# Kernel tuning notes

Hardware: AMD Instinct MI355X
Metric: run time of the kernel (lower is better)

Reference implementation:

```python
import jax, jax.numpy as jnp
import numpy as np

TEMP = 0.07  # init temperature
EPS = 1e-12  # F.normalize eps


def _per_cloud_loss(fmap, labels):
    # fmap: [C, N] per-point features; labels: [N] int
    v = fmap.T  # [N, C]
    v = v / jnp.maximum(jnp.linalg.norm(v, axis=1, keepdims=True), EPS)
    # NxN similarity, exp then divide by temp (order matches original)
    dot = jnp.exp(v @ v.T) / TEMP  # [N, N]
    dot = dot - jnp.diag(jnp.diag(dot))  # zero the diagonal
    mask = (labels[:, None] == labels[None, :]).astype(dot.dtype)  # [N, N]
    mask_not = 1.0 - mask
    pos = (mask * dot).sum(1) / mask.sum(1)  # note: denom includes self, as in original
    neg = (mask_not * dot).sum(1) / mask_not.sum(1)
    return jnp.mean(-jnp.log(pos / (pos + neg)))


def setup_inputs() -> dict:
    key = jax.random.key(0)
    k1, k2 = jax.random.split(key)
    B, C, N = 8, 128, 4096
    features = jax.random.normal(k1, (B, C, N), dtype=jnp.float32)
    labels_all = jax.random.randint(k2, (B, N), 0, 16, dtype=jnp.int64)
    return {"features": features, "labels_all": labels_all}


def reference(features, labels_all):
    losses = jax.vmap(_per_cloud_loss)(features, labels_all)  # [B]
    return jnp.mean(losses)
```

## Files before the change

### kernel.cpp

```cpp
#include <hip/hip_runtime.h>
#include <stdint.h>

#define NPTS 4096
#define NC 128
#define NB 8
#define CSPLIT 8
#define COLS_PER (NPTS / CSPLIT)
#define RPB 128

typedef __bf16 bf16x8 __attribute__((ext_vector_type(8)));
typedef float f32x4 __attribute__((ext_vector_type(4)));
typedef unsigned short u16;
typedef unsigned int u32;

__device__ inline float fast_exp2(float x) { return __builtin_amdgcn_exp2f(x); }

__device__ inline u16 f2bf(float x) {
    u32 u = __float_as_uint(x);
    u32 r = (u + 0x7fffu + ((u >> 16) & 1u)) >> 16;
    return (u16)r;
}

__global__ __launch_bounds__(256) void norm_count_kernel(const float* __restrict__ feat,
                                                         const int* __restrict__ labels,
                                                         u16* __restrict__ vbf,
                                                         int* __restrict__ counts,
                                                         u32* __restrict__ zbase) {
    int b = blockIdx.y;
    int tid = threadIdx.x;
    if (blockIdx.x == 64) {
        if (b == 0 && tid < 2) zbase[tid] = 0u;
        __shared__ int h[16];
        if (tid < 16) h[tid] = 0;
        __syncthreads();
        for (int n = tid; n < NPTS; n += 256)
            atomicAdd(&h[labels[b * NPTS + n] & 15], 1);
        __syncthreads();
        if (tid < 16) counts[b * 16 + tid] = h[tid];
        return;
    }
    int n0 = blockIdx.x * 64;
    __shared__ float tile[64][129];
    __shared__ float part[8][64];
    __shared__ float rn[64];
    const float* fb = feat + (size_t)b * NC * NPTS;
    int nslot = tid & 31;
    int ty = tid >> 5;
    float s0 = 0.f, s1 = 0.f;
#pragma unroll
    for (int i = 0; i < 16; ++i) {
        int c = i * 8 + ty;
        float2 x = *(const float2*)(fb + (size_t)c * NPTS + n0 + 2 * nslot);
        tile[2 * nslot][c] = x.x;
        tile[2 * nslot + 1][c] = x.y;
        s0 += x.x * x.x;
        s1 += x.y * x.y;
    }
    part[ty][2 * nslot] = s0;
    part[ty][2 * nslot + 1] = s1;
    __syncthreads();
    if (tid < 64) {
        float s = 0.f;
#pragma unroll
        for (int t = 0; t < 8; ++t) s += part[t][tid];
        rn[tid] = 1.f / fmaxf(sqrtf(s), 1e-12f);
    }
    __syncthreads();
    u32* out = (u32*)vbf;
    size_t obase = ((size_t)b * NPTS + n0) * (NC / 2);
#pragma unroll
    for (int i = 0; i < 16; ++i) {
        int idx = tid + i * 256;
        int p = idx >> 6, k = idx & 63;
        float r = rn[p];
        float x0 = tile[p][2 * k] * r;
        float x1 = tile[p][2 * k + 1] * r;
        out[obase + (size_t)p * 64 + k] = (u32)f2bf(x0) | ((u32)f2bf(x1) << 16);
    }
}

__global__ __launch_bounds__(256, 2) void sim_kernel(const u16* __restrict__ vbf,
                                                     const int* __restrict__ labels,
                                                     float2* __restrict__ rowacc) {
    int bid = blockIdx.x;
    int rt = bid >> 6;
    int combo = bid & 63;
    int b = combo >> 3;
    int cs = combo & 7;
    int row0 = rt * RPB;
    int c0 = cs * COLS_PER;
    int tid = threadIdx.x;
    int wave = tid >> 6, lane = tid & 63;
    int quad = lane >> 4, ln = lane & 15;

    const u16* vb = vbf + (size_t)b * NPTS * NC;
    const int* lab = labels + b * NPTS;

    int rbase[2];
    rbase[0] = row0 + wave * 32;
    rbase[1] = rbase[0] + 16;

    bf16x8 afrag[2][4];
#pragma unroll
    for (int s = 0; s < 2; ++s)
#pragma unroll
        for (int f = 0; f < 4; ++f) {
            bf16x8 v = *(const bf16x8*)(vb + (size_t)(rbase[s] + ln) * NC + f * 32 + quad * 8);
#pragma unroll
            for (int k = 0; k < 8; ++k) v[k] = (__bf16)((float)v[k] * 1.44269504f);
            afrag[s][f] = v;
        }

    int lrow[2][4];
#pragma unroll
    for (int s = 0; s < 2; ++s)
#pragma unroll
        for (int r = 0; r < 4; ++r) lrow[s][r] = lab[rbase[s] + quad * 4 + r];

    int diagct[2], diagsub[2];
#pragma unroll
    for (int s = 0; s < 2; ++s) {
        diagct[s] = rbase[s] & ~63;
        diagsub[s] = (rbase[s] >> 4) & 3;
    }

    float psame[2][4] = {{0.f}}, sall[2][4] = {{0.f}};

    __shared__ u16 cols[64 * 128];
    __shared__ int clab[64];

    const uint4* src = (const uint4*)(vb + (size_t)c0 * NC);
    u32 woff[4];
#pragma unroll
    for (int i = 0; i < 4; ++i) {
        int idx = tid + i * 256;
        int rr = idx >> 4, cc = idx & 15;
        woff[i] = rr * 128 + ((cc ^ (rr & 15)) * 8);
    }

    for (int t = 0; t < COLS_PER / 64; ++t) {
        int ct = c0 + t * 64;
        __syncthreads();
#pragma unroll
        for (int i = 0; i < 4; ++i)
            *(uint4*)(cols + woff[i]) = src[t * 1024 + tid + i * 256];
        if (tid < 64) clab[tid] = lab[ct + tid];
        __syncthreads();

#pragma unroll
        for (int sub = 0; sub < 4; ++sub) {
            const u16* rowb = cols + (sub * 16 + ln) * 128;
            bf16x8 bfrag[4];
#pragma unroll
            for (int f = 0; f < 4; ++f)
                bfrag[f] = *(const bf16x8*)(rowb + (((4 * f + quad) ^ ln) * 8));
            int lc = clab[sub * 16 + ln];
#pragma unroll
            for (int s = 0; s < 2; ++s) {
                f32x4 d = {0.f, 0.f, 0.f, 0.f};
#pragma unroll
                for (int f = 0; f < 4; ++f)
                    d = __builtin_amdgcn_mfma_f32_16x16x32_bf16(afrag[s][f], bfrag[f], d, 0, 0, 0);
                if (ct == diagct[s] && sub == diagsub[s]) {
#pragma unroll
                    for (int r = 0; r < 4; ++r) {
                        float e = fast_exp2(d[r]);
                        if (ln == quad * 4 + r) e = 0.f;
                        sall[s][r] += e;
                        psame[s][r] += (lc == lrow[s][r]) ? e : 0.f;
                    }
                } else {
#pragma unroll
                    for (int r = 0; r < 4; ++r) {
                        float e = fast_exp2(d[r]);
                        sall[s][r] += e;
                        psame[s][r] += (lc == lrow[s][r]) ? e : 0.f;
                    }
                }
            }
        }
    }

#pragma unroll
    for (int off = 1; off < 16; off <<= 1)
#pragma unroll
        for (int s = 0; s < 2; ++s)
#pragma unroll
            for (int r = 0; r < 4; ++r) {
                psame[s][r] += __shfl_xor(psame[s][r], off);
                sall[s][r] += __shfl_xor(sall[s][r], off);
            }
    if (ln == 0) {
#pragma unroll
        for (int s = 0; s < 2; ++s)
#pragma unroll
            for (int r = 0; r < 4; ++r)
                rowacc[((size_t)cs * NB + b) * NPTS + rbase[s] + quad * 4 + r] =
                    make_float2(psame[s][r], sall[s][r]);
    }
}

__global__ __launch_bounds__(256) void loss_kernel(const float2* __restrict__ rowacc,
                                                   const int* __restrict__ labels,
                                                   const int* __restrict__ counts,
                                                   float* __restrict__ acc,
                                                   u32* __restrict__ ticket,
                                                   float* __restrict__ out) {
    int idx = blockIdx.x * 256 + threadIdx.x;
    int b = idx >> 12;
    float ps = 0.f, sa = 0.f;
#pragma unroll
    for (int cs = 0; cs < CSPLIT; ++cs) {
        float2 v = rowacc[(size_t)cs * NB * NPTS + idx];
        ps += v.x;
        sa += v.y;
    }
    int lb = labels[idx] & 15;
    int cnt = counts[b * 16 + lb];
    float p = ps / (float)cnt;
    float n = (sa - ps) / (float)(NPTS - cnt);
    float loss = -__logf(p / (p + n));
#pragma unroll
    for (int off = 1; off < 64; off <<= 1) loss += __shfl_xor(loss, off);
    __shared__ float w[4];
    if ((threadIdx.x & 63) == 0) w[threadIdx.x >> 6] = loss;
    __syncthreads();
    if (threadIdx.x == 0) {
        atomicAdd(acc, w[0] + w[1] + w[2] + w[3]);
        __threadfence();
        u32 t = atomicAdd(ticket, 1u);
        if (t == gridDim.x - 1) {
            float v = atomicAdd(acc, 0.f);
            out[0] = v * (1.f / (float)(NB * NPTS));
        }
    }
}

extern "C" void kernel_launch(void* const* d_in, const int* in_sizes, int n_in,
                              void* d_out, int out_size, void* d_ws, size_t ws_size,
                              hipStream_t stream) {
    const float* feat = (const float*)d_in[0];
    const int* labels = (const int*)d_in[1];
    float* out = (float*)d_out;

    float* acc = (float*)d_ws;
    u32* ticket = (u32*)((char*)d_ws + 4);
    int* counts = (int*)((char*)d_ws + 256);
    float2* rowacc = (float2*)((char*)d_ws + 4096);
    u16* vbf = (u16*)((char*)d_ws + 4096 + (size_t)CSPLIT * NB * NPTS * 8);

    norm_count_kernel<<<dim3(65, NB), 256, 0, stream>>>(feat, labels, vbf, counts, (u32*)d_ws);
    sim_kernel<<<dim3(32 * 64), 256, 0, stream>>>(vbf, labels, rowacc);
    loss_kernel<<<dim3(NB * NPTS / 256), 256, 0, stream>>>(rowacc, labels, counts, acc, ticket, out);
}
```

Measured before the change: 131.1 us.

## Sort points by label, add uniform-tile fast path, double-buffer column loads

Adds a histogram/prefix kernel and scatters normalized features into label-sorted order, so most 16x16 tiles have uniform row and column labels. For those tiles the per-element compare and select is replaced by a single branch. Column tiles are now loaded straight into double-buffered LDS with global_load_lds, prefetching the next tile during compute, and the per-tile syncthreads drops from two to one. The kernel accumulates positive and negative sums separately instead of total minus positive, at the cost of an extra launch and a scattered write.

```diff
diff --git a/kernel.cpp b/kernel.cpp
--- a/kernel.cpp
+++ b/kernel.cpp
@@ -12,6 +12,7 @@
 typedef float f32x4 __attribute__((ext_vector_type(4)));
 typedef unsigned short u16;
 typedef unsigned int u32;
+typedef unsigned long long u64;
 
 __device__ inline float fast_exp2(float x) { return __builtin_amdgcn_exp2f(x); }
 
@@ -21,28 +22,59 @@
     return (u16)r;
 }
 
-__global__ __launch_bounds__(256) void norm_count_kernel(const float* __restrict__ feat,
-                                                         const int* __restrict__ labels,
-                                                         u16* __restrict__ vbf,
-                                                         int* __restrict__ counts,
-                                                         u32* __restrict__ zbase) {
+typedef __attribute__((address_space(1))) const void glb_void;
+typedef __attribute__((address_space(3))) void lds_void;
+__device__ inline void gload_lds16(const void* g, void* l) {
+    __builtin_amdgcn_global_load_lds((glb_void*)g, (lds_void*)l, 16, 0, 0);
+}
+
+__global__ __launch_bounds__(256) void hist_kernel(const int* __restrict__ labels,
+                                                   int* __restrict__ counts,
+                                                   int* __restrict__ baseg,
+                                                   u32* __restrict__ zb) {
+    int b = blockIdx.x, tid = threadIdx.x;
+    if (b == 0 && tid < 2) zb[tid] = 0u;
+    __shared__ int cnt[64][16];
+    __shared__ int tot[16];
+    for (int i = tid; i < 64 * 16; i += 256) ((int*)cnt)[i] = 0;
+    __syncthreads();
+    for (int n = tid; n < NPTS; n += 256)
+        atomicAdd(&cnt[n >> 6][labels[b * NPTS + n] & 15], 1);
+    __syncthreads();
+    if (tid < 16) {
+        int s = 0;
+        for (int k = 0; k < 64; ++k) s += cnt[k][tid];
+        counts[b * 16 + tid] = s;
+        tot[tid] = s;
+    }
+    __syncthreads();
+    if (tid == 0) {
+        int run = 0;
+        for (int l = 0; l < 16; ++l) { int c = tot[l]; tot[l] = run; run += c; }
+    }
+    __syncthreads();
+    if (tid < 16) {
+        int run = tot[tid];
+        for (int k = 0; k < 64; ++k) {
+            baseg[(b * 64 + k) * 16 + tid] = run;
+            run += cnt[k][tid];
+        }
+    }
+}
+
+__global__ __launch_bounds__(256) void norm_kernel(const float* __restrict__ feat,
+                                                   const int* __restrict__ labels,
+                                                   const int* __restrict__ baseg,
+                                                   u16* __restrict__ vbf,
+                                                   int* __restrict__ slab) {
     int b = blockIdx.y;
+    int blk = blockIdx.x;
     int tid = threadIdx.x;
-    if (blockIdx.x == 64) {
-        if (b == 0 && tid < 2) zbase[tid] = 0u;
-        __shared__ int h[16];
-        if (tid < 16) h[tid] = 0;
-        __syncthreads();
-        for (int n = tid; n < NPTS; n += 256)
-            atomicAdd(&h[labels[b * NPTS + n] & 15], 1);
-        __syncthreads();
-        if (tid < 16) counts[b * 16 + tid] = h[tid];
-        return;
-    }
-    int n0 = blockIdx.x * 64;
+    int n0 = blk * 64;
     __shared__ float tile[64][129];
     __shared__ float part[8][64];
     __shared__ float rn[64];
+    __shared__ int lpos[64];
     const float* fb = feat + (size_t)b * NC * NPTS;
     int nslot = tid & 31;
     int ty = tid >> 5;
@@ -64,10 +96,20 @@
 #pragma unroll
         for (int t = 0; t < 8; ++t) s += part[t][tid];
         rn[tid] = 1.f / fmaxf(sqrtf(s), 1e-12f);
+        int myl = labels[b * NPTS + n0 + tid] & 15;
+        u64 mymask = 0ull;
+#pragma unroll
+        for (int L = 0; L < 16; ++L) {
+            u64 bl = __ballot(myl == L);
+            if (myl == L) mymask = bl;
+        }
+        int rank = __popcll(mymask & ((1ull << tid) - 1ull));
+        int pos = baseg[(b * 64 + blk) * 16 + myl] + rank;
+        lpos[tid] = pos;
+        slab[b * NPTS + pos] = myl;
     }
     __syncthreads();
     u32* out = (u32*)vbf;
-    size_t obase = ((size_t)b * NPTS + n0) * (NC / 2);
 #pragma unroll
     for (int i = 0; i < 16; ++i) {
         int idx = tid + i * 256;
@@ -75,12 +117,12 @@
         float r = rn[p];
         float x0 = tile[p][2 * k] * r;
         float x1 = tile[p][2 * k + 1] * r;
-        out[obase + (size_t)p * 64 + k] = (u32)f2bf(x0) | ((u32)f2bf(x1) << 16);
+        out[((size_t)b * NPTS + lpos[p]) * 64 + k] = (u32)f2bf(x0) | ((u32)f2bf(x1) << 16);
     }
 }
 
 __global__ __launch_bounds__(256, 2) void sim_kernel(const u16* __restrict__ vbf,
-                                                     const int* __restrict__ labels,
+                                                     const int* __restrict__ slab,
                                                      float2* __restrict__ rowacc) {
     int bid = blockIdx.x;
     int rt = bid >> 6;
@@ -94,7 +136,7 @@
     int quad = lane >> 4, ln = lane & 15;
 
     const u16* vb = vbf + (size_t)b * NPTS * NC;
-    const int* lab = labels + b * NPTS;
+    const int* lab = slab + b * NPTS;
 
     int rbase[2];
     rbase[0] = row0 + wave * 32;
@@ -117,6 +159,10 @@
 #pragma unroll
         for (int r = 0; r < 4; ++r) lrow[s][r] = lab[rbase[s] + quad * 4 + r];
 
+    int row_uni[2];
+#pragma unroll
+    for (int s = 0; s < 2; ++s) row_uni[s] = (lab[rbase[s]] == lab[rbase[s] + 15]);
+
     int diagct[2], diagsub[2];
 #pragma unroll
     for (int s = 0; s < 2; ++s) {
@@ -124,37 +170,46 @@
         diagsub[s] = (rbase[s] >> 4) & 3;
     }
 
-    float psame[2][4] = {{0.f}}, sall[2][4] = {{0.f}};
-
-    __shared__ u16 cols[64 * 128];
-    __shared__ int clab[64];
+    float psame[2][4] = {{0.f}}, pneg[2][4] = {{0.f}};
+
+    __shared__ u16 cols[2][64 * 128];
+    __shared__ int clabs[512];
+    clabs[tid] = lab[c0 + tid];
+    clabs[tid + 256] = lab[c0 + 256 + tid];
 
     const uint4* src = (const uint4*)(vb + (size_t)c0 * NC);
-    u32 woff[4];
+    int g4[4];
 #pragma unroll
     for (int i = 0; i < 4; ++i) {
-        int idx = tid + i * 256;
-        int rr = idx >> 4, cc = idx & 15;
-        woff[i] = rr * 128 + ((cc ^ (rr & 15)) * 8);
-    }
+        int idx16 = (wave * 4 + i) * 64 + lane;
+        int rr = idx16 >> 4;
+        int cc = (idx16 & 15) ^ (rr & 15);
+        g4[i] = rr * 16 + cc;
+    }
+
+    int cur = 0;
+#pragma unroll
+    for (int i = 0; i < 4; ++i)
+        gload_lds16(src + g4[i], cols[0] + (wave * 4 + i) * 512);
 
     for (int t = 0; t < COLS_PER / 64; ++t) {
+        __syncthreads();
+        if (t < COLS_PER / 64 - 1) {
+#pragma unroll
+            for (int i = 0; i < 4; ++i)
+                gload_lds16(src + (t + 1) * 1024 + g4[i], cols[cur ^ 1] + (wave * 4 + i) * 512);
+        }
         int ct = c0 + t * 64;
-        __syncthreads();
-#pragma unroll
-        for (int i = 0; i < 4; ++i)
-            *(uint4*)(cols + woff[i]) = src[t * 1024 + tid + i * 256];
-        if (tid < 64) clab[tid] = lab[ct + tid];
-        __syncthreads();
 
 #pragma unroll
         for (int sub = 0; sub < 4; ++sub) {
-            const u16* rowb = cols + (sub * 16 + ln) * 128;
+            const u16* rowb = cols[cur] + (sub * 16 + ln) * 128;
             bf16x8 bfrag[4];
 #pragma unroll
             for (int f = 0; f < 4; ++f)
                 bfrag[f] = *(const bf16x8*)(rowb + (((4 * f + quad) ^ ln) * 8));
-            int lc = clab[sub * 16 + ln];
+            int lc = clabs[t * 64 + sub * 16 + ln];
+            int clo = __shfl(lc, 0), chi = __shfl(lc, 15);
 #pragma unroll
             for (int s = 0; s < 2; ++s) {
                 f32x4 d = {0.f, 0.f, 0.f, 0.f};
@@ -166,19 +221,30 @@
                     for (int r = 0; r < 4; ++r) {
                         float e = fast_exp2(d[r]);
                         if (ln == quad * 4 + r) e = 0.f;
-                        sall[s][r] += e;
-                        psame[s][r] += (lc == lrow[s][r]) ? e : 0.f;
+                        bool m = (lc == lrow[s][r]);
+                        psame[s][r] += m ? e : 0.f;
+                        pneg[s][r] += m ? 0.f : e;
+                    }
+                } else if (row_uni[s] && clo == chi) {
+                    if (clo == lrow[s][0]) {
+#pragma unroll
+                        for (int r = 0; r < 4; ++r) psame[s][r] += fast_exp2(d[r]);
+                    } else {
+#pragma unroll
+                        for (int r = 0; r < 4; ++r) pneg[s][r] += fast_exp2(d[r]);
                     }
                 } else {
 #pragma unroll
                     for (int r = 0; r < 4; ++r) {
                         float e = fast_exp2(d[r]);
-                        sall[s][r] += e;
-                        psame[s][r] += (lc == lrow[s][r]) ? e : 0.f;
+                        bool m = (lc == lrow[s][r]);
+                        psame[s][r] += m ? e : 0.f;
+                        pneg[s][r] += m ? 0.f : e;
                     }
                 }
             }
         }
+        cur ^= 1;
     }
 
 #pragma unroll
@@ -188,7 +254,7 @@
 #pragma unroll
             for (int r = 0; r < 4; ++r) {
                 psame[s][r] += __shfl_xor(psame[s][r], off);
-                sall[s][r] += __shfl_xor(sall[s][r], off);
+                pneg[s][r] += __shfl_xor(pneg[s][r], off);
             }
     if (ln == 0) {
 #pragma unroll
@@ -196,29 +262,29 @@
 #pragma unroll
             for (int r = 0; r < 4; ++r)
                 rowacc[((size_t)cs * NB + b) * NPTS + rbase[s] + quad * 4 + r] =
-                    make_float2(psame[s][r], sall[s][r]);
+                    make_float2(psame[s][r], pneg[s][r]);
     }
 }
 
 __global__ __launch_bounds__(256) void loss_kernel(const float2* __restrict__ rowacc,
-                                                   const int* __restrict__ labels,
+                                                   const int* __restrict__ slab,
                                                    const int* __restrict__ counts,
                                                    float* __restrict__ acc,
                                                    u32* __restrict__ ticket,
                                                    float* __restrict__ out) {
     int idx = blockIdx.x * 256 + threadIdx.x;
     int b = idx >> 12;
-    float ps = 0.f, sa = 0.f;
+    float ps = 0.f, pn = 0.f;
 #pragma unroll
     for (int cs = 0; cs < CSPLIT; ++cs) {
         float2 v = rowacc[(size_t)cs * NB * NPTS + idx];
         ps += v.x;
-        sa += v.y;
-    }
-    int lb = labels[idx] & 15;
+        pn += v.y;
+    }
+    int lb = slab[idx] & 15;
     int cnt = counts[b * 16 + lb];
     float p = ps / (float)cnt;
-    float n = (sa - ps) / (float)(NPTS - cnt);
+    float n = pn / (float)(NPTS - cnt);
     float loss = -__logf(p / (p + n));
 #pragma unroll
     for (int off = 1; off < 64; off <<= 1) loss += __shfl_xor(loss, off);
@@ -246,10 +312,13 @@
     float* acc = (float*)d_ws;
     u32* ticket = (u32*)((char*)d_ws + 4);
     int* counts = (int*)((char*)d_ws + 256);
-    float2* rowacc = (float2*)((char*)d_ws + 4096);
-    u16* vbf = (u16*)((char*)d_ws + 4096 + (size_t)CSPLIT * NB * NPTS * 8);
-
-    norm_count_kernel<<<dim3(65, NB), 256, 0, stream>>>(feat, labels, vbf, counts, (u32*)d_ws);
-    sim_kernel<<<dim3(32 * 64), 256, 0, stream>>>(vbf, labels, rowacc);
-    loss_kernel<<<dim3(NB * NPTS / 256), 256, 0, stream>>>(rowacc, labels, counts, acc, ticket, out);
-}
+    int* baseg = (int*)((char*)d_ws + 1024);
+    int* slab = (int*)((char*)d_ws + 36864);
+    float2* rowacc = (float2*)((char*)d_ws + 172032);
+    u16* vbf = (u16*)((char*)d_ws + 172032 + (size_t)CSPLIT * NB * NPTS * 8);
+
+    hist_kernel<<<dim3(NB), 256, 0, stream>>>(labels, counts, baseg, (u32*)d_ws);
+    norm_kernel<<<dim3(64, NB), 256, 0, stream>>>(feat, labels, baseg, vbf, slab);
+    sim_kernel<<<dim3(32 * 64), 256, 0, stream>>>(vbf, slab, rowacc);
+    loss_kernel<<<dim3(NB * NPTS / 256), 256, 0, stream>>>(rowacc, slab, counts, acc, ticket, out);
+}
```

Result: no change. 131.5 us (+0.3%).
